# Kernel tuning notes

Measured on AMD Instinct MI355X. Metric: run time of the kernel, lower is better.

Reference implementation:

```python
import jax, jax.numpy as jnp
import numpy as np

EPS = 1e-8  # torch CosineSimilarity eps


def _neg_indices(N):
    # boolean mask removing diag and the +/-N diagonals, then per-row column
    # indices of the surviving (negative) entries: shape (2N, 2N-2)
    two_n = 2 * N
    mask = ~(np.eye(two_n, dtype=bool)
             | np.eye(two_n, k=N, dtype=bool)
             | np.eye(two_n, k=-N, dtype=bool))
    rows, cols = np.nonzero(mask)  # row-major order matches torch bool indexing
    return cols.reshape(two_n, two_n - 2)


def setup_inputs() -> dict:
    key = jax.random.key(0)
    k1, k2 = jax.random.split(key)
    B, D = 4096, 128
    return {
        "zis": jax.random.normal(k1, (B, D), dtype=jnp.float32),
        "zjs": jax.random.normal(k2, (B, D), dtype=jnp.float32),
    }


def reference(zis, zjs):
    N = zis.shape[0]
    temperature = 0.5
    reps = jnp.concatenate([zjs, zis], axis=0)            # (2N, D)
    norms = jnp.maximum(jnp.linalg.norm(reps, axis=-1, keepdims=True), EPS)
    r = reps / norms
    sim = r @ r.T                                         # (2N, 2N) cosine sims
    l_pos = jnp.diagonal(sim, offset=N)                   # (N,)
    r_pos = jnp.diagonal(sim, offset=-N)                  # (N,)
    positives = jnp.concatenate([l_pos, r_pos])[:, None]  # (2N, 1)
    neg_idx = jnp.asarray(_neg_indices(N))                # (2N, 2N-2) static
    negatives = jnp.take_along_axis(sim, neg_idx, axis=1) # (2N, 2N-2)
    logits = jnp.concatenate([positives, negatives], axis=1) / temperature
    # CrossEntropy with labels all 0, reduction='sum'
    loss = -jnp.sum(jax.nn.log_softmax(logits, axis=-1)[:, 0])
    return loss / (2 * N)
```

## Files before the change

kernel.cpp:

```cpp
#include <hip/hip_runtime.h>
#include <hip/hip_bf16.h>
#include <stdint.h>

typedef __attribute__((ext_vector_type(8))) short bf16x8;
typedef __attribute__((ext_vector_type(4))) float f32x4;

#define TWO_N 8192
#define NHALF 4096
#define DIM   128

#define SQRT_C 1.69864361f
#define LN2    0.69314718055994531f

__device__ __forceinline__ unsigned int f2bf(float f) {
  unsigned int u = __float_as_uint(f);
  u += 0x7FFFu + ((u >> 16) & 1u);
  return u >> 16;
}

__global__ __launch_bounds__(256) void norm_kernel(
    const float* __restrict__ zis, const float* __restrict__ zjs,
    unsigned int* __restrict__ rbf ) {
  const int wave = threadIdx.x >> 6;
  const int lane = threadIdx.x & 63;
  const int row = blockIdx.x * 4 + wave;
  const float* src = (row < NHALF) ? (zjs + (size_t)row * DIM)
                                   : (zis + (size_t)(row - NHALF) * DIM);
  float2 v = ((const float2*)src)[lane];
  float ss = v.x * v.x + v.y * v.y;
#pragma unroll
  for (int m = 1; m <= 32; m <<= 1) ss += __shfl_xor(ss, m);
  const float scale = SQRT_C / fmaxf(sqrtf(ss), 1e-8f);
  const unsigned int lo = f2bf(v.x * scale);
  const unsigned int hi = f2bf(v.y * scale);
  rbf[(size_t)row * (DIM / 2) + lane] = lo | (hi << 16);
}

#define GLL16(SRC, DST) __builtin_amdgcn_global_load_lds( \
    (__attribute__((address_space(1))) void*)(SRC),       \
    (__attribute__((address_space(3))) void*)(DST), 16, 0, 0)

#define STAGE128(ROWBASE, DST) do {                                        \
  _Pragma("unroll")                                                        \
  for (int i_ = 0; i_ < 8; ++i_) {                                         \
    const int L_ = (i_ * 256 + t) * 16;                                    \
    const int row_ = L_ >> 8;                                              \
    const int cb_ = L_ & 255;                                              \
    GLL16(rbytes + (size_t)((ROWBASE) + row_) * 256 +                      \
              (cb_ ^ ((row_ & 7) << 4)),                                   \
          (DST) + L_);                                                     \
  }                                                                        \
} while (0)

__global__ __launch_bounds__(256)
__attribute__((amdgpu_waves_per_eu(2, 2)))
void simloss_kernel(
    char* __restrict__ rbytes,
    float* __restrict__ pos,
    float* __restrict__ s_part) {
  __shared__ char Ab[32768];
  __shared__ char Bb[32768];
  const int t = threadIdx.x;
  const int rb = blockIdx.x >> 3;
  const int cs = blockIdx.x & 7;
  const int RB = rb * 128;
  const int CS = cs * 1024;
  const int wave = t >> 6;
  const int lane = t & 63;
  const int wr = wave >> 1, wc = wave & 1;
  const int lrow = lane >> 4, lcol = lane & 15;

  STAGE128(RB, Ab);
  STAGE128(CS, Bb);
  __syncthreads();

  bf16x8 a_reg[4][4];
#pragma unroll
  for (int ks = 0; ks < 4; ++ks)
#pragma unroll
    for (int m = 0; m < 4; ++m) {
      const int row = wr * 64 + m * 16 + lcol;
      const int kb = ks * 64 + lrow * 16;
      a_reg[ks][m] = *(const bf16x8*)(Ab + row * 256 + (kb ^ ((row & 7) << 4)));
    }
  __syncthreads();

  float srun[4][4];
#pragma unroll
  for (int m = 0; m < 4; ++m)
#pragma unroll
    for (int r = 0; r < 4; ++r) srun[m][r] = 0.0f;

  char* curB = Bb;
  char* nxtB = Ab;
#pragma unroll 1
  for (int ct = 0; ct < 8; ++ct) {
    if (ct < 7) STAGE128(CS + (ct + 1) * 128, nxtB);

    const int CB = CS + ct * 128;
    f32x4 acc[4][4];
#pragma unroll
    for (int m = 0; m < 4; ++m)
#pragma unroll
      for (int n = 0; n < 4; ++n) acc[m][n] = (f32x4){0.f, 0.f, 0.f, 0.f};

#pragma unroll
    for (int ks = 0; ks < 4; ++ks) {
      bf16x8 bfr[4];
#pragma unroll
      for (int n = 0; n < 4; ++n) {
        const int row = wc * 64 + n * 16 + lcol;
        const int kb = ks * 64 + lrow * 16;
        bfr[n] = *(const bf16x8*)(curB + row * 256 + (kb ^ ((row & 7) << 4)));
      }
#pragma unroll
      for (int m = 0; m < 4; ++m)
#pragma unroll
        for (int n = 0; n < 4; ++n)
          acc[m][n] = __builtin_amdgcn_mfma_f32_16x16x32_bf16(
              a_reg[ks][m], bfr[n], acc[m][n], 0, 0, 0);
    }

#pragma unroll
    for (int m = 0; m < 4; ++m) {
      const int R0 = RB + wr * 64 + m * 16;
#pragma unroll
      for (int n = 0; n < 4; ++n) {
        const int C0 = CB + wc * 64 + n * 16;
        const bool hasDiag = (C0 == R0);
        const bool hasPartner = (C0 == (R0 ^ 4096));
#pragma unroll
        for (int r = 0; r < 4; ++r) {
          const float v = acc[m][n][r];
          float e = __builtin_amdgcn_exp2f(v);
          const bool mine = (lcol == lrow * 4 + r);
          if (hasPartner && mine) pos[R0 + lrow * 4 + r] = v;
          if (hasDiag && mine) e = 0.0f;
          srun[m][r] += e;
        }
      }
    }
    __syncthreads();
    char* tmp = curB; curB = nxtB; nxtB = tmp;
  }

#pragma unroll
  for (int m = 0; m < 4; ++m)
#pragma unroll
    for (int r = 0; r < 4; ++r) {
      float s = srun[m][r];
      s += __shfl_xor(s, 1);
      s += __shfl_xor(s, 2);
      s += __shfl_xor(s, 4);
      s += __shfl_xor(s, 8);
      if (lcol == 0)
        s_part[(size_t)(cs * 2 + wc) * TWO_N +
               (RB + wr * 64 + m * 16 + lrow * 4 + r)] = s;
    }
}

__global__ __launch_bounds__(256) void reduce1_kernel(
    const float* __restrict__ pos, const float* __restrict__ s_part,
    float* __restrict__ partial) {
  const int t = threadIdx.x;
  const int row = blockIdx.x * 256 + t;
  float s = 0.0f;
#pragma unroll
  for (int q = 0; q < 16; ++q) s += s_part[(size_t)q * TWO_N + row];
  float local = (__log2f(s) - pos[row]) * LN2;
#pragma unroll
  for (int m = 1; m <= 32; m <<= 1) local += __shfl_xor(local, m);
  __shared__ float wsum[4];
  if ((t & 63) == 0) wsum[t >> 6] = local;
  __syncthreads();
  if (t == 0) partial[blockIdx.x] = wsum[0] + wsum[1] + wsum[2] + wsum[3];
}

__global__ __launch_bounds__(64) void reduce2_kernel(
    const float* __restrict__ partial, float* __restrict__ out) {
  float v = (threadIdx.x < 32) ? partial[threadIdx.x] : 0.0f;
#pragma unroll
  for (int m = 1; m <= 32; m <<= 1) v += __shfl_xor(v, m);
  if (threadIdx.x == 0) out[0] = v * (1.0f / TWO_N);
}

extern "C" void kernel_launch(void* const* d_in, const int* in_sizes, int n_in,
                              void* d_out, int out_size, void* d_ws, size_t ws_size,
                              hipStream_t stream) {
  const float* zis = (const float*)d_in[0];
  const float* zjs = (const float*)d_in[1];
  char* ws = (char*)d_ws;
  unsigned int* rbf = (unsigned int*)ws;
  float* pos = (float*)(ws + 2u * 1024 * 1024);
  float* s_part = (float*)(ws + 2u * 1024 * 1024 + 32 * 1024);
  float* partial = (float*)(ws + 2u * 1024 * 1024 + 32 * 1024 + 512 * 1024);

  norm_kernel<<<TWO_N / 4, 256, 0, stream>>>(zis, zjs, rbf);
  simloss_kernel<<<512, 256, 0, stream>>>((char*)rbf, pos, s_part);
  reduce1_kernel<<<TWO_N / 256, 256, 0, stream>>>(pos, s_part, partial);
  reduce2_kernel<<<1, 64, 0, stream>>>(partial, (float*)d_out);
}
```

Before: 85.89 us.

## Exploit symmetry of similarity matrix to compute only upper-triangle tiles

Since sim is symmetric, each block now processes a contiguous range of upper-triangular 128x128 tiles (2080 tiles split over 512 blocks) and emits both row sums and column sums per tile. This roughly halves the MFMA and exp work. The reduction kernel now sums 128 partial slices instead of 16, so the workspace grows. The cost is per-tile shuffle reductions, more s_part writes, and an extra A reload with a synchronisation whenever the tile row changes.

```diff
diff --git a/kernel.cpp b/kernel.cpp
--- a/kernel.cpp
+++ b/kernel.cpp
@@ -52,52 +52,64 @@
   }                                                                        \
 } while (0)
 
+#define HOIST_A(SRCBUF) do {                                               \
+  _Pragma("unroll")                                                        \
+  for (int ks_ = 0; ks_ < 4; ++ks_)                                        \
+    _Pragma("unroll")                                                      \
+    for (int m_ = 0; m_ < 4; ++m_) {                                       \
+      const int row_ = wr * 64 + m_ * 16 + lcol;                           \
+      const int kb_ = ks_ * 64 + lrow * 16;                                \
+      a_reg[ks_][m_] = *(const bf16x8*)((SRCBUF) + row_ * 256 +            \
+                                        (kb_ ^ ((row_ & 7) << 4)));        \
+    }                                                                      \
+} while (0)
+
 __global__ __launch_bounds__(256)
 __attribute__((amdgpu_waves_per_eu(2, 2)))
 void simloss_kernel(
     char* __restrict__ rbytes,
     float* __restrict__ pos,
     float* __restrict__ s_part) {
-  __shared__ char Ab[32768];
-  __shared__ char Bb[32768];
+  __shared__ char Buf0[32768];
+  __shared__ char Buf1[32768];
   const int t = threadIdx.x;
-  const int rb = blockIdx.x >> 3;
-  const int cs = blockIdx.x & 7;
-  const int RB = rb * 128;
-  const int CS = cs * 1024;
+  const int b = blockIdx.x;
+  const int Tstart = (65 * b) >> 4;
+  const int Tend = (65 * (b + 1)) >> 4;
   const int wave = t >> 6;
   const int lane = t & 63;
   const int wr = wave >> 1, wc = wave & 1;
   const int lrow = lane >> 4, lcol = lane & 15;
 
-  STAGE128(RB, Ab);
-  STAGE128(CS, Bb);
+  int ci = (int)((129.0f - sqrtf((float)(16641 - 8 * Tstart))) * 0.5f);
+  if (ci > 63) ci = 63;
+  while ((ci + 1) * (129 - (ci + 1)) / 2 <= Tstart) ++ci;
+  while (ci * (129 - ci) / 2 > Tstart) --ci;
+  int cj = ci + (Tstart - ci * (129 - ci) / 2);
+
+  STAGE128(ci * 128, Buf0);
+  STAGE128(cj * 128, Buf1);
   __syncthreads();
 
   bf16x8 a_reg[4][4];
-#pragma unroll
-  for (int ks = 0; ks < 4; ++ks)
-#pragma unroll
-    for (int m = 0; m < 4; ++m) {
-      const int row = wr * 64 + m * 16 + lcol;
-      const int kb = ks * 64 + lrow * 16;
-      a_reg[ks][m] = *(const bf16x8*)(Ab + row * 256 + (kb ^ ((row & 7) << 4)));
-    }
+  HOIST_A(Buf0);
   __syncthreads();
 
-  float srun[4][4];
-#pragma unroll
-  for (int m = 0; m < 4; ++m)
-#pragma unroll
-    for (int r = 0; r < 4; ++r) srun[m][r] = 0.0f;
-
-  char* curB = Bb;
-  char* nxtB = Ab;
+  char* curB = Buf1;
+  char* nxtB = Buf0;
+
 #pragma unroll 1
-  for (int ct = 0; ct < 8; ++ct) {
-    if (ct < 7) STAGE128(CS + (ct + 1) * 128, nxtB);
-
-    const int CB = CS + ct * 128;
+  for (int q = Tstart; q < Tend; ++q) {
+    const int i = ci, j = cj;
+    const bool more = (q + 1 < Tend);
+    const bool sw = (j == 63);
+    const int in1 = sw ? i + 1 : i;
+    const int jn1 = sw ? i + 1 : j + 1;
+    if (more) {
+      if (!sw) STAGE128(jn1 * 128, nxtB);
+      else     STAGE128(in1 * 128, nxtB);
+    }
+
     f32x4 acc[4][4];
 #pragma unroll
     for (int m = 0; m < 4; ++m)
@@ -121,42 +133,78 @@
               a_reg[ks][m], bfr[n], acc[m][n], 0, 0, 0);
     }
 
+    const bool diag_tile = (i == j);
+    const bool partner_tile = (j == i + 32);
+    float rsum[4][4];
+    float csum[4];
+#pragma unroll
+    for (int m = 0; m < 4; ++m)
+#pragma unroll
+      for (int r = 0; r < 4; ++r) rsum[m][r] = 0.0f;
+#pragma unroll
+    for (int n = 0; n < 4; ++n) csum[n] = 0.0f;
+
 #pragma unroll
     for (int m = 0; m < 4; ++m) {
-      const int R0 = RB + wr * 64 + m * 16;
 #pragma unroll
       for (int n = 0; n < 4; ++n) {
-        const int C0 = CB + wc * 64 + n * 16;
-        const bool hasDiag = (C0 == R0);
-        const bool hasPartner = (C0 == (R0 ^ 4096));
+        const bool onsub = (wc == wr) && (n == m);
 #pragma unroll
         for (int r = 0; r < 4; ++r) {
           const float v = acc[m][n][r];
           float e = __builtin_amdgcn_exp2f(v);
-          const bool mine = (lcol == lrow * 4 + r);
-          if (hasPartner && mine) pos[R0 + lrow * 4 + r] = v;
-          if (hasDiag && mine) e = 0.0f;
-          srun[m][r] += e;
+          const bool mine = onsub && (lcol == lrow * 4 + r);
+          if (partner_tile && mine) {
+            const int row = i * 128 + wr * 64 + m * 16 + lrow * 4 + r;
+            pos[row] = v;
+            pos[row + 4096] = v;
+          }
+          if (diag_tile && mine) e = 0.0f;
+          rsum[m][r] += e;
+          csum[n] += e;
         }
       }
     }
+
+#pragma unroll
+    for (int m = 0; m < 4; ++m)
+#pragma unroll
+      for (int r = 0; r < 4; ++r) {
+        float s = rsum[m][r];
+        s += __shfl_xor(s, 1);
+        s += __shfl_xor(s, 2);
+        s += __shfl_xor(s, 4);
+        s += __shfl_xor(s, 8);
+        if (lcol == 0)
+          s_part[(size_t)(2 * j + wc) * TWO_N +
+                 (i * 128 + wr * 64 + m * 16 + lrow * 4 + r)] = s;
+      }
+
+    if (!diag_tile) {
+#pragma unroll
+      for (int n = 0; n < 4; ++n) {
+        float c = csum[n];
+        c += __shfl_xor(c, 16);
+        c += __shfl_xor(c, 32);
+        if (lrow == 0)
+          s_part[(size_t)(2 * i + wr) * TWO_N +
+                 (j * 128 + wc * 64 + n * 16 + lcol)] = c;
+      }
+    }
+
     __syncthreads();
-    char* tmp = curB; curB = nxtB; nxtB = tmp;
+
+    if (more) {
+      if (!sw) {
+        char* tmp = curB; curB = nxtB; nxtB = tmp;
+      } else {
+        HOIST_A(nxtB);
+        STAGE128(jn1 * 128, curB);
+        __syncthreads();
+      }
+      ci = in1; cj = jn1;
+    }
   }
-
-#pragma unroll
-  for (int m = 0; m < 4; ++m)
-#pragma unroll
-    for (int r = 0; r < 4; ++r) {
-      float s = srun[m][r];
-      s += __shfl_xor(s, 1);
-      s += __shfl_xor(s, 2);
-      s += __shfl_xor(s, 4);
-      s += __shfl_xor(s, 8);
-      if (lcol == 0)
-        s_part[(size_t)(cs * 2 + wc) * TWO_N +
-               (RB + wr * 64 + m * 16 + lrow * 4 + r)] = s;
-    }
 }
 
 __global__ __launch_bounds__(256) void reduce1_kernel(
@@ -165,8 +213,8 @@
   const int t = threadIdx.x;
   const int row = blockIdx.x * 256 + t;
   float s = 0.0f;
-#pragma unroll
-  for (int q = 0; q < 16; ++q) s += s_part[(size_t)q * TWO_N + row];
+#pragma unroll 8
+  for (int q = 0; q < 128; ++q) s += s_part[(size_t)q * TWO_N + row];
   float local = (__log2f(s) - pos[row]) * LN2;
 #pragma unroll
   for (int m = 1; m <= 32; m <<= 1) local += __shfl_xor(local, m);
@@ -193,7 +241,7 @@
   unsigned int* rbf = (unsigned int*)ws;
   float* pos = (float*)(ws + 2u * 1024 * 1024);
   float* s_part = (float*)(ws + 2u * 1024 * 1024 + 32 * 1024);
-  float* partial = (float*)(ws + 2u * 1024 * 1024 + 32 * 1024 + 512 * 1024);
+  float* partial = (float*)(ws + 6u * 1024 * 1024 + 32 * 1024);
 
   norm_kernel<<<TWO_N / 4, 256, 0, stream>>>(zis, zjs, rbf);
   simloss_kernel<<<512, 256, 0, stream>>>((char*)rbf, pos, s_part);
```

Result: slower. 96.33 us (+12.2%).

## Load MFMA operands directly from global memory instead of LDS staging

Applied to the files above, without the earlier changes.

Removes the LDS double-buffered staging of A and B tiles and has each wave load its bf16 fragments straight from global memory (L2/L1), dropping all block-level barriers in the column loop. The B fragments for a whole 128-column tile are loaded into registers up front. This aims to remove LDS traffic and synchronisation, at the cost of redundant global loads across waves that share the same B rows, higher register pressure, and exposed load latency with no explicit prefetch.

```diff
diff --git a/kernel.cpp b/kernel.cpp
--- a/kernel.cpp
+++ b/kernel.cpp
@@ -36,30 +36,12 @@
   rbf[(size_t)row * (DIM / 2) + lane] = lo | (hi << 16);
 }
 
-#define GLL16(SRC, DST) __builtin_amdgcn_global_load_lds( \
-    (__attribute__((address_space(1))) void*)(SRC),       \
-    (__attribute__((address_space(3))) void*)(DST), 16, 0, 0)
-
-#define STAGE128(ROWBASE, DST) do {                                        \
-  _Pragma("unroll")                                                        \
-  for (int i_ = 0; i_ < 8; ++i_) {                                         \
-    const int L_ = (i_ * 256 + t) * 16;                                    \
-    const int row_ = L_ >> 8;                                              \
-    const int cb_ = L_ & 255;                                              \
-    GLL16(rbytes + (size_t)((ROWBASE) + row_) * 256 +                      \
-              (cb_ ^ ((row_ & 7) << 4)),                                   \
-          (DST) + L_);                                                     \
-  }                                                                        \
-} while (0)
-
 __global__ __launch_bounds__(256)
 __attribute__((amdgpu_waves_per_eu(2, 2)))
 void simloss_kernel(
-    char* __restrict__ rbytes,
+    const char* __restrict__ rbytes,
     float* __restrict__ pos,
     float* __restrict__ s_part) {
-  __shared__ char Ab[32768];
-  __shared__ char Bb[32768];
   const int t = threadIdx.x;
   const int rb = blockIdx.x >> 3;
   const int cs = blockIdx.x & 7;
@@ -70,20 +52,14 @@
   const int wr = wave >> 1, wc = wave & 1;
   const int lrow = lane >> 4, lcol = lane & 15;
 
-  STAGE128(RB, Ab);
-  STAGE128(CS, Bb);
-  __syncthreads();
-
   bf16x8 a_reg[4][4];
 #pragma unroll
   for (int ks = 0; ks < 4; ++ks)
 #pragma unroll
-    for (int m = 0; m < 4; ++m) {
-      const int row = wr * 64 + m * 16 + lcol;
-      const int kb = ks * 64 + lrow * 16;
-      a_reg[ks][m] = *(const bf16x8*)(Ab + row * 256 + (kb ^ ((row & 7) << 4)));
-    }
-  __syncthreads();
+    for (int m = 0; m < 4; ++m)
+      a_reg[ks][m] = *(const bf16x8*)(
+          rbytes + (size_t)(RB + wr * 64 + m * 16 + lcol) * 256 +
+          ks * 64 + lrow * 16);
 
   float srun[4][4];
 #pragma unroll
@@ -91,13 +67,19 @@
 #pragma unroll
     for (int r = 0; r < 4; ++r) srun[m][r] = 0.0f;
 
-  char* curB = Bb;
-  char* nxtB = Ab;
+  const char* bptr = rbytes + (size_t)(CS + wc * 64 + lcol) * 256 + lrow * 16;
+
 #pragma unroll 1
   for (int ct = 0; ct < 8; ++ct) {
-    if (ct < 7) STAGE128(CS + (ct + 1) * 128, nxtB);
+    const int CB = CS + ct * 128;
 
-    const int CB = CS + ct * 128;
+    bf16x8 bfr[4][4];
+#pragma unroll
+    for (int n = 0; n < 4; ++n)
+#pragma unroll
+      for (int ks = 0; ks < 4; ++ks)
+        bfr[ks][n] = *(const bf16x8*)(bptr + n * 4096 + ks * 64);
+
     f32x4 acc[4][4];
 #pragma unroll
     for (int m = 0; m < 4; ++m)
@@ -105,21 +87,13 @@
       for (int n = 0; n < 4; ++n) acc[m][n] = (f32x4){0.f, 0.f, 0.f, 0.f};
 
 #pragma unroll
-    for (int ks = 0; ks < 4; ++ks) {
-      bf16x8 bfr[4];
-#pragma unroll
-      for (int n = 0; n < 4; ++n) {
-        const int row = wc * 64 + n * 16 + lcol;
-        const int kb = ks * 64 + lrow * 16;
-        bfr[n] = *(const bf16x8*)(curB + row * 256 + (kb ^ ((row & 7) << 4)));
-      }
+    for (int ks = 0; ks < 4; ++ks)
 #pragma unroll
       for (int m = 0; m < 4; ++m)
 #pragma unroll
         for (int n = 0; n < 4; ++n)
           acc[m][n] = __builtin_amdgcn_mfma_f32_16x16x32_bf16(
-              a_reg[ks][m], bfr[n], acc[m][n], 0, 0, 0);
-    }
+              a_reg[ks][m], bfr[ks][n], acc[m][n], 0, 0, 0);
 
 #pragma unroll
     for (int m = 0; m < 4; ++m) {
@@ -140,8 +114,7 @@
         }
       }
     }
-    __syncthreads();
-    char* tmp = curB; curB = nxtB; nxtB = tmp;
+    bptr += 32768;
   }
 
 #pragma unroll
@@ -193,10 +166,10 @@
   unsigned int* rbf = (unsigned int*)ws;
   float* pos = (float*)(ws + 2u * 1024 * 1024);
   float* s_part = (float*)(ws + 2u * 1024 * 1024 + 32 * 1024);
-  float* partial = (float*)(ws + 2u * 1024 * 1024 + 32 * 1024 + 512 * 1024);
+  float* partial = (float*)(ws + 2u * 1024 * 1024 + 544 * 1024);
 
   norm_kernel<<<TWO_N / 4, 256, 0, stream>>>(zis, zjs, rbf);
-  simloss_kernel<<<512, 256, 0, stream>>>((char*)rbf, pos, s_part);
+  simloss_kernel<<<512, 256, 0, stream>>>((const char*)rbf, pos, s_part);
   reduce1_kernel<<<TWO_N / 256, 256, 0, stream>>>(pos, s_part, partial);
   reduce2_kernel<<<1, 64, 0, stream>>>(partial, (float*)d_out);
 }
```

Measured after the change: 99.75 us. +16.1%, slower.
